# Optimization experiments

Measured on AMD Instinct MI355X. Metric: run time of the kernel, lower is better.

Reference implementation:

```python
import jax, jax.numpy as jnp
import numpy as np

B, T, D = 128, 2048, 256


def setup_inputs() -> dict:
    key = jax.random.key(0)
    ks = jax.random.split(key, 6)
    s = 1.0 / np.sqrt(D)  # kaiming-uniform-ish scale for bias-free Linear
    return {
        "x": jax.random.normal(ks[0], (B, T, D), jnp.float32),
        "W_in": jax.random.normal(ks[1], (D, D), jnp.float32) * s,
        "W_select": jax.random.normal(ks[2], (D, D), jnp.float32) * s,
        "W_gate": jax.random.normal(ks[3], (D, D), jnp.float32) * s,
        "W_out": jax.random.normal(ks[4], (D, D), jnp.float32) * s,
        "W_delta": jax.random.normal(ks[5], (D, D), jnp.float32) * s,
        "log_a": jnp.zeros((D,), jnp.float32),  # module inits log_a = zeros
    }


def _diag_recurrence(decay, update):
    # state_t = decay_t * state_{t-1} + update_t, state_{-1} = 0 (zero-init fast path)
    # First-order linear recurrence as an associative scan:
    # (a1,b1) o (a2,b2) = (a1*a2, a2*b1 + b2)
    def combine(c1, c2):
        a1, b1 = c1
        a2, b2 = c2
        return a1 * a2, a2 * b1 + b2

    _, states = jax.lax.associative_scan(combine, (decay, update), axis=1)
    return states  # (B, T, D)


def reference(x, W_in, W_select, W_gate, W_out, W_delta, log_a):
    # selective diag-SSM (a_mode='diag'):
    #   delta  = softplus(delta_proj(x))                  timestep / selectivity
    #   decay  = exp(-delta * exp(log_a))                 in (0, 1]
    #   update = delta * sigmoid(select_proj(x)) * in_proj(x)
    #   states = scan(state = decay*state + update)
    #   y      = states * silu(gate_proj(x)); out = out_proj(y)
    delta = jax.nn.softplus(jnp.einsum("btd,ed->bte", x, W_delta))
    decay = jnp.exp(-delta * jnp.exp(log_a))
    u = jnp.einsum("btd,ed->bte", x, W_in)
    sel = jax.nn.sigmoid(jnp.einsum("btd,ed->bte", x, W_select))
    update = delta * sel * u
    states = _diag_recurrence(decay, update)
    gate = jax.nn.silu(jnp.einsum("btd,ed->bte", x, W_gate))
    return jnp.einsum("btd,ed->bte", states * gate, W_out)
```

## Files before the change

### kernel.cpp

```cpp
#include <hip/hip_runtime.h>
#include <hip/hip_bf16.h>
#include <hip/hip_fp16.h>
#include <math.h>


typedef __attribute__((ext_vector_type(8))) short s16x8;
typedef __attribute__((ext_vector_type(4))) float f32x4;

#define D_DIM 256
#define T_DIM 2048
#define B_DIM 128
#define NCHUNK2 32
#define CLEN 128
#define BK 64

__device__ __forceinline__ unsigned short f2bf(float f) {
    union { float f; unsigned int u; } v; v.f = f;
    unsigned int r = v.u + 0x7fffu + ((v.u >> 16) & 1u);
    return (unsigned short)(r >> 16);
}
__device__ __forceinline__ float bf2f(unsigned short s) {
    union { unsigned int u; float f; } v; v.u = ((unsigned int)s) << 16;
    return v.f;
}
__device__ __forceinline__ void gload_lds16(const void* g, void* l) {
    __builtin_amdgcn_global_load_lds(
        (const __attribute__((address_space(1))) unsigned int*)g,
        (__attribute__((address_space(3))) unsigned int*)l, 16, 0, 0);
}

__global__ __launch_bounds__(256) void prep_kernel(
    const float* __restrict__ W_in, const float* __restrict__ W_select,
    const float* __restrict__ W_gate, const float* __restrict__ W_out,
    const float* __restrict__ W_delta, const float* __restrict__ log_a,
    unsigned short* __restrict__ Wb, float* __restrict__ ea)
{
    int i = blockIdx.x * 256 + threadIdx.x;
    if (i < 4 * 65536) {
        int row = i >> 8, k = i & 255;
        int n = row >> 2, w = row & 3;
        const float* src = (w == 0) ? W_delta : (w == 1) ? W_select
                         : (w == 2) ? W_in    : W_gate;
        Wb[i] = f2bf(src[n * 256 + k]);
    } else if (i < 5 * 65536) {
        Wb[i] = f2bf(W_out[i - 4 * 65536]);
    } else if (i < 5 * 65536 + 256) {
        int j = i - 5 * 65536;
        ea[j] = expf(log_a[j]);
    }
}

__global__ __launch_bounds__(256) void xcast_kernel(
    const float* __restrict__ x, unsigned short* __restrict__ xb)
{
    size_t i = ((size_t)blockIdx.x * 256 + threadIdx.x) * 8;
    float4 p0 = *(const float4*)(x + i);
    float4 p1 = *(const float4*)(x + i + 4);
    s16x8 a;
    a[0] = (short)f2bf(p0.x); a[1] = (short)f2bf(p0.y);
    a[2] = (short)f2bf(p0.z); a[3] = (short)f2bf(p0.w);
    a[4] = (short)f2bf(p1.x); a[5] = (short)f2bf(p1.y);
    a[6] = (short)f2bf(p1.z); a[7] = (short)f2bf(p1.w);
    *(s16x8*)(xb + i) = a;
}

__global__ __launch_bounds__(256, 3) void gemm_fused_kernel(
    const unsigned short* __restrict__ xb, const unsigned short* __restrict__ Wcat,
    const float* __restrict__ ea,
    __half2* __restrict__ du, unsigned short* __restrict__ gate,
    float* __restrict__ cA, float* __restrict__ cS)
{
    __shared__ char lds[32768];
    int bid = blockIdx.x;
    int wg  = (bid & 7) * 2048 + (bid >> 3);
    int mt  = wg >> 3;
    int nt  = wg & 7;
    int mbase = mt * 128;
    int nb = nt * 128;
    int tid = threadIdx.x, lane = tid & 63, wid = tid >> 6;
    int l16 = lane & 15, lk = lane >> 4;
    int wr = wid >> 1, wc = wid & 1;
    int srow = tid >> 3;
    int sgi  = tid & 7;

    f32x4 acc[4][4] = {};

    for (int ks = 0; ks < 4; ++ks) {
        int kb = ks * BK;
#pragma unroll
        for (int j = 0; j < 4; ++j) {
            int row = j * 32 + srow;
            int sg  = sgi ^ (row & 7);
            gload_lds16(xb + (size_t)(mbase + row) * D_DIM + kb + sg * 8,
                        lds + row * 128 + sgi * 16);
        }
#pragma unroll
        for (int j = 0; j < 4; ++j) {
            int row = j * 32 + srow;
            int sg  = sgi ^ (row & 7);
            gload_lds16(Wcat + (size_t)(nb + row) * D_DIM + kb + sg * 8,
                        lds + 16384 + row * 128 + sgi * 16);
        }
        __syncthreads();

#pragma unroll
        for (int kk = 0; kk < 2; ++kk) {
            int gp = ((kk * 4 + lk) ^ (l16 & 7)) * 16;
            s16x8 xf[4], wf[4];
#pragma unroll
            for (int mf = 0; mf < 4; ++mf)
                xf[mf] = *(const s16x8*)(lds
                           + (wr * 64 + mf * 16 + l16) * 128 + gp);
#pragma unroll
            for (int nf = 0; nf < 4; ++nf)
                wf[nf] = *(const s16x8*)(lds + 16384
                           + (wc * 64 + nf * 16 + l16) * 128 + gp);
#pragma unroll
            for (int nf = 0; nf < 4; ++nf)
#pragma unroll
                for (int mf = 0; mf < 4; ++mf)
                    acc[mf][nf] = __builtin_amdgcn_mfma_f32_16x16x32_bf16(
                        wf[nf], xf[mf], acc[mf][nf], 0, 0, 0);
        }
        __syncthreads();
    }

#pragma unroll
    for (int nf = 0; nf < 4; ++nf) {
        int dl = wc * 16 + nf * 4 + lk;
        float ean = ea[nt * 32 + dl];
        float A[4], S[4];
#pragma unroll
        for (int mf = 0; mf < 4; ++mf) {
            int t = wr * 64 + mf * 16 + l16;
            float zd = acc[mf][nf][0];
            float zs = acc[mf][nf][1];
            float zi = acc[mf][nf][2];
            float zg = acc[mf][nf][3];
            float e = __expf(zd);
            float delta = (zd > 15.f) ? zd : __logf(1.f + e);
            float dec = __expf(-delta * ean);
            float sel = 1.f / (1.f + __expf(-zs));
            float upd = delta * sel * zi;
            float g   = zg / (1.f + __expf(-zg));
            *(__half2*)(lds + (t * 36 + dl) * 4) = __floats2half2_rn(dec, upd);
            *(unsigned short*)(lds + 18432 + t * 80 + dl * 2) = f2bf(g);
            A[mf] = dec;
            S[mf] = upd;
        }
#pragma unroll
        for (int d = 1; d < 16; d <<= 1) {
            bool upper = (l16 & d);
#pragma unroll
            for (int mf = 0; mf < 4; ++mf) {
                float Ap = __shfl_xor(A[mf], d, 64);
                float Sp = __shfl_xor(S[mf], d, 64);
                float Se = upper ? Sp : S[mf];
                float Al = upper ? A[mf] : Ap;
                float Sl = upper ? S[mf] : Sp;
                S[mf] = fmaf(Al, Se, Sl);
                A[mf] = A[mf] * Ap;
            }
        }
        float cAe = A[0], cSe = S[0];
#pragma unroll
        for (int mf = 1; mf < 4; ++mf) {
            cSe = fmaf(A[mf], cSe, S[mf]);
            cAe *= A[mf];
        }
        if (l16 == 0) {
            int hc = mt * 2 + wr;
            cA[hc * D_DIM + nt * 32 + dl] = cAe;
            cS[hc * D_DIM + nt * 32 + dl] = cSe;
        }
    }
    __syncthreads();

    {
        size_t dub = (size_t)mbase * D_DIM + nt * 32;
#pragma unroll
        for (int i = 0; i < 4; ++i) {
            int slot = i * 256 + tid;
            int t = slot >> 3, seg = slot & 7;
            f32x4 v = *(const f32x4*)(lds + t * 144 + seg * 16);
            *(f32x4*)(du + dub + (size_t)t * D_DIM + seg * 4) = v;
        }
#pragma unroll
        for (int i = 0; i < 2; ++i) {
            int slot = i * 256 + tid;
            int t = slot >> 2, seg = slot & 3;
            f32x4 v = *(const f32x4*)(lds + 18432 + t * 80 + seg * 16);
            *(f32x4*)(gate + dub + (size_t)t * D_DIM + seg * 8) = v;
        }
    }
}

__global__ __launch_bounds__(256) void scan2_kernel(
    const float* __restrict__ cA, const float* __restrict__ cS,
    float* __restrict__ carry)
{
    int b = blockIdx.x;
    int d = threadIdx.x;
    float s = 0.f;
    for (int c = 0; c < NCHUNK2; ++c) {
        int idx = (b * NCHUNK2 + c) * D_DIM + d;
        carry[idx] = s;
        s = fmaf(cA[idx], s, cS[idx]);
    }
}

__global__ __launch_bounds__(256) void scan_out_kernel(
    const __half2* __restrict__ du, const unsigned short* __restrict__ gate,
    const float* __restrict__ carry, const unsigned short* __restrict__ Wo,
    float* __restrict__ out)
{
    __shared__ unsigned short yls[128 * 256];
    int b = blockIdx.x >> 4;
    int c = blockIdx.x & 15;
    int tid = threadIdx.x;

    {
        int d = tid;
        size_t base = ((size_t)b * T_DIM + (size_t)c * CLEN) * D_DIM + d;
        float s = carry[(b * NCHUNK2 + c * 2) * D_DIM + d];
        int dlo = d & 7, dch = d >> 3;
#pragma unroll 4
        for (int t = 0; t < CLEN; ++t) {
            __half2 v = du[base + (size_t)t * D_DIM];
            float dc = __low2float(v);
            float up = __high2float(v);
            s = fmaf(dc, s, up);
            float g = bf2f(gate[base + (size_t)t * D_DIM]);
            int off = t * 256 + ((dch ^ (t & 7)) << 3) + dlo;
            yls[off] = f2bf(s * g);
        }
    }
    __syncthreads();

    int lane = tid & 63, wid = tid >> 6;
    int l16 = lane & 15;
    int lkc = lane >> 4;
    int m0 = (wid >> 1) * 64;
    size_t rbase = (size_t)b * T_DIM + (size_t)c * CLEN;
    int r0 = lkc * 4;

    for (int nblk = 0; nblk < 2; ++nblk) {
        int n0 = (wid & 1) * 64 + nblk * 128;
        f32x4 acc[4][4] = {};
        for (int ks = 0; ks < 8; ++ks) {
            int kb = ks * 32 + lkc * 8;
            s16x8 yf[4];
#pragma unroll
            for (int mf = 0; mf < 4; ++mf) {
                int row = m0 + mf * 16 + l16;
                int chunk = (ks * 4 + lkc) ^ (row & 7);
                yf[mf] = *(const s16x8*)&yls[row * 256 + chunk * 8];
            }
#pragma unroll
            for (int nf = 0; nf < 4; ++nf) {
                s16x8 wfr = *(const s16x8*)(Wo + (size_t)(n0 + nf * 16 + l16) * D_DIM + kb);
#pragma unroll
                for (int mf = 0; mf < 4; ++mf)
                    acc[mf][nf] = __builtin_amdgcn_mfma_f32_16x16x32_bf16(
                        wfr, yf[mf], acc[mf][nf], 0, 0, 0);
            }
        }
#pragma unroll
        for (int mf = 0; mf < 4; ++mf) {
            size_t rowg = rbase + m0 + mf * 16 + l16;
#pragma unroll
            for (int nf = 0; nf < 4; ++nf) {
                int n = n0 + nf * 16 + r0;
                *(f32x4*)(out + rowg * D_DIM + n) = acc[mf][nf];
            }
        }
    }
}

extern "C" void kernel_launch(void* const* d_in, const int* in_sizes, int n_in,
                              void* d_out, int out_size, void* d_ws, size_t ws_size,
                              hipStream_t stream)
{
    const float* x        = (const float*)d_in[0];
    const float* W_in     = (const float*)d_in[1];
    const float* W_select = (const float*)d_in[2];
    const float* W_gate   = (const float*)d_in[3];
    const float* W_out    = (const float*)d_in[4];
    const float* W_delta  = (const float*)d_in[5];
    const float* log_a    = (const float*)d_in[6];
    float* out = (float*)d_out;

    char* ws = (char*)d_ws;
    const size_t MB = 1ull << 20;
    unsigned short* Wb    = (unsigned short*)(ws);
    float*          ea    = (float*)(ws + 655360);
    unsigned short* xb    = (unsigned short*)(ws + 1 * MB);
    __half2*        du    = (__half2*)(ws + 129 * MB);
    unsigned short* gate  = (unsigned short*)(ws + 385 * MB);
    float*          cA    = (float*)(ws + 513 * MB);
    float*          cS    = (float*)(ws + 517 * MB);
    float*          carry = (float*)(ws + 521 * MB);

    prep_kernel<<<1281, 256, 0, stream>>>(W_in, W_select, W_gate, W_out,
                                          W_delta, log_a, Wb, ea);
    xcast_kernel<<<32768, 256, 0, stream>>>(x, xb);
    gemm_fused_kernel<<<16384, 256, 0, stream>>>(xb, Wb, ea, du, gate, cA, cS);
    scan2_kernel<<<B_DIM, 256, 0, stream>>>(cA, cS, carry);
    scan_out_kernel<<<B_DIM * NCHUNK2 / 2, 256, 0, stream>>>(du, gate, carry,
                                                             Wb + 4 * 65536, out);
}
```

Measured before the change: 592.3 us.

## Load full-K weight tile into LDS once and stream x fragments from global

The GEMM kernel now stages the whole 128x256 weight slice into a 64KB LDS buffer in one pass, instead of looping over four K-steps with a barrier each. The x operand fragments are read straight from global memory into registers and double-buffered (A/B sets), so the loads for the next K slice overlap the current MFMA block. This removes the per-step barriers and the LDS round-trip for x. In exchange it doubles LDS use, lowers the occupancy hint from 3 to 2 blocks, and makes x reads uncoalesced per lane, which may raise global memory latency.

```diff
diff --git a/kernel.cpp b/kernel.cpp
--- a/kernel.cpp
+++ b/kernel.cpp
@@ -12,7 +12,6 @@
 #define B_DIM 128
 #define NCHUNK2 32
 #define CLEN 128
-#define BK 64
 
 __device__ __forceinline__ unsigned short f2bf(float f) {
     union { float f; unsigned int u; } v; v.f = f;
@@ -64,13 +63,13 @@
     *(s16x8*)(xb + i) = a;
 }
 
-__global__ __launch_bounds__(256, 3) void gemm_fused_kernel(
+__global__ __launch_bounds__(256, 2) void gemm_fused_kernel(
     const unsigned short* __restrict__ xb, const unsigned short* __restrict__ Wcat,
     const float* __restrict__ ea,
     __half2* __restrict__ du, unsigned short* __restrict__ gate,
     float* __restrict__ cA, float* __restrict__ cS)
 {
-    __shared__ char lds[32768];
+    __shared__ char lds[65536];
     int bid = blockIdx.x;
     int wg  = (bid & 7) * 2048 + (bid >> 3);
     int mt  = wg >> 3;
@@ -80,50 +79,70 @@
     int tid = threadIdx.x, lane = tid & 63, wid = tid >> 6;
     int l16 = lane & 15, lk = lane >> 4;
     int wr = wid >> 1, wc = wid & 1;
-    int srow = tid >> 3;
-    int sgi  = tid & 7;
+
+#pragma unroll
+    for (int j = 0; j < 16; ++j) {
+        int e = j * 256 + tid;
+        int row = e >> 5, gsl = e & 31;
+        int g = gsl ^ (row & 7);
+        gload_lds16(Wcat + (size_t)(nb + row) * D_DIM + g * 8,
+                    lds + e * 16);
+    }
+
+    const unsigned short* xrow =
+        xb + (size_t)(mbase + wr * 64 + l16) * D_DIM + lk * 8;
+
+    s16x8 xfA[4], xfB[4], wfA[4], wfB[4];
+#pragma unroll
+    for (int mf = 0; mf < 4; ++mf)
+        xfA[mf] = *(const s16x8*)(xrow + mf * 16 * D_DIM);
+
+    __syncthreads();
+
+    int wrow[4];
+#pragma unroll
+    for (int nf = 0; nf < 4; ++nf)
+        wrow[nf] = (wc * 64 + nf * 16 + l16) * 512;
+    int wsw = ((wc * 64 + l16) & 7);
+
+#pragma unroll
+    for (int nf = 0; nf < 4; ++nf)
+        wfA[nf] = *(const s16x8*)(lds + wrow[nf] + ((lk ^ wsw) * 16));
 
     f32x4 acc[4][4] = {};
 
-    for (int ks = 0; ks < 4; ++ks) {
-        int kb = ks * BK;
-#pragma unroll
-        for (int j = 0; j < 4; ++j) {
-            int row = j * 32 + srow;
-            int sg  = sgi ^ (row & 7);
-            gload_lds16(xb + (size_t)(mbase + row) * D_DIM + kb + sg * 8,
-                        lds + row * 128 + sgi * 16);
-        }
-#pragma unroll
-        for (int j = 0; j < 4; ++j) {
-            int row = j * 32 + srow;
-            int sg  = sgi ^ (row & 7);
-            gload_lds16(Wcat + (size_t)(nb + row) * D_DIM + kb + sg * 8,
-                        lds + 16384 + row * 128 + sgi * 16);
-        }
-        __syncthreads();
-
-#pragma unroll
-        for (int kk = 0; kk < 2; ++kk) {
-            int gp = ((kk * 4 + lk) ^ (l16 & 7)) * 16;
-            s16x8 xf[4], wf[4];
+#pragma unroll
+    for (int k2 = 0; k2 < 4; ++k2) {
+        int kkO = 2 * k2 + 1;
+#pragma unroll
+        for (int mf = 0; mf < 4; ++mf)
+            xfB[mf] = *(const s16x8*)(xrow + mf * 16 * D_DIM + kkO * 32);
+#pragma unroll
+        for (int nf = 0; nf < 4; ++nf)
+            wfB[nf] = *(const s16x8*)(lds + wrow[nf] + (((kkO * 4 + lk) ^ wsw) * 16));
+#pragma unroll
+        for (int nf = 0; nf < 4; ++nf)
 #pragma unroll
             for (int mf = 0; mf < 4; ++mf)
-                xf[mf] = *(const s16x8*)(lds
-                           + (wr * 64 + mf * 16 + l16) * 128 + gp);
+                acc[mf][nf] = __builtin_amdgcn_mfma_f32_16x16x32_bf16(
+                    wfA[nf], xfA[mf], acc[mf][nf], 0, 0, 0);
+        if (k2 < 3) {
+            int kkE = 2 * k2 + 2;
+#pragma unroll
+            for (int mf = 0; mf < 4; ++mf)
+                xfA[mf] = *(const s16x8*)(xrow + mf * 16 * D_DIM + kkE * 32);
 #pragma unroll
             for (int nf = 0; nf < 4; ++nf)
-                wf[nf] = *(const s16x8*)(lds + 16384
-                           + (wc * 64 + nf * 16 + l16) * 128 + gp);
-#pragma unroll
-            for (int nf = 0; nf < 4; ++nf)
-#pragma unroll
-                for (int mf = 0; mf < 4; ++mf)
-                    acc[mf][nf] = __builtin_amdgcn_mfma_f32_16x16x32_bf16(
-                        wf[nf], xf[mf], acc[mf][nf], 0, 0, 0);
-        }
-        __syncthreads();
-    }
+                wfA[nf] = *(const s16x8*)(lds + wrow[nf] + (((kkE * 4 + lk) ^ wsw) * 16));
+        }
+#pragma unroll
+        for (int nf = 0; nf < 4; ++nf)
+#pragma unroll
+            for (int mf = 0; mf < 4; ++mf)
+                acc[mf][nf] = __builtin_amdgcn_mfma_f32_16x16x32_bf16(
+                    wfB[nf], xfB[mf], acc[mf][nf], 0, 0, 0);
+    }
+    __syncthreads();
 
 #pragma unroll
     for (int nf = 0; nf < 4; ++nf) {
```

Measured after the change: 728.1 us. +22.9%, slower.
